# Kernel optimization log

Measured on AMD Instinct MI355X. Metric: run time of the kernel, lower is better.

Reference implementation:

```python
import jax, jax.numpy as jnp
import numpy as np

_SIGMA = 1.5
_K1 = 0.01
_K2 = 0.03
_WINDOW_SIZE = 11
_N_CHANNELS = 3
_VALUE_RANGE = 1.0
_WEIGHTS = np.array([0.0448, 0.2856, 0.3001, 0.2363, 0.1333], dtype=np.float32)


def create_window(window_size: int, n_channels: int) -> jnp.ndarray:
    # 2D Gaussian kernel, normalized to sum 1, expanded to depthwise (C,1,ws,ws)
    coords = np.arange(window_size, dtype=np.float32) - (window_size - 1) / 2.0
    g = np.exp(-(coords ** 2) / (2.0 * _SIGMA ** 2))
    g = g / g.sum()
    k2d = np.outer(g, g).astype(np.float32)  # (ws, ws), sums to 1
    window = np.broadcast_to(k2d[None, None], (n_channels, 1, window_size, window_size))
    return jnp.asarray(window)


def _dwconv(x, window):
    # depthwise valid conv, NCHW / OIHW
    c = x.shape[1]
    return jax.lax.conv_general_dilated(
        x, window, window_strides=(1, 1), padding='VALID',
        dimension_numbers=('NCHW', 'OIHW', 'NCHW'), feature_group_count=c)


def _avg_pool2(x):
    # torch F.avg_pool2d(kernel=2, stride=2, padding=(H%2, W%2), count_include_pad=True)
    ph = x.shape[-2] % 2
    pw = x.shape[-1] % 2
    s = jax.lax.reduce_window(
        x, 0.0, jax.lax.add, window_dimensions=(1, 1, 2, 2),
        window_strides=(1, 1, 2, 2), padding=((0, 0), (0, 0), (ph, ph), (pw, pw)))
    return s * 0.25


def ssim_per_channel(x, y, window, value_range):
    mu_x = _dwconv(x, window)
    mu_y = _dwconv(y, window)
    mu_x_sq = mu_x ** 2
    mu_y_sq = mu_y ** 2
    mu_xy = mu_x * mu_y
    sigma_x_sq = _dwconv(x * x, window) - mu_x_sq
    sigma_y_sq = _dwconv(y * y, window) - mu_y_sq
    sigma_xy = _dwconv(x * y, window) - mu_xy
    c1 = (_K1 * value_range) ** 2
    c2 = (_K2 * value_range) ** 2
    cs_map = (2.0 * sigma_xy + c2) / (sigma_x_sq + sigma_y_sq + c2)
    ssim_map = (2.0 * mu_xy + c1) / (mu_x_sq + mu_y_sq + c1) * cs_map
    return ssim_map.mean(axis=(-1, -2)), cs_map.mean(axis=(-1, -2))  # (N, C) each


def msssim_per_channel(x, y, window, weights, value_range):
    n_scales = weights.shape[0]
    mcs = []
    for i in range(n_scales):
        if i > 0:
            x = _avg_pool2(x)
            y = _avg_pool2(y)
        ssim_val, cs = ssim_per_channel(x, y, window, value_range)
        mcs.append(jax.nn.relu(cs))
    stacked = jnp.stack(mcs[:-1] + [ssim_val], axis=0)  # (M, N, C)
    stacked = stacked ** weights[:, None, None]
    return jnp.prod(stacked, axis=0)  # (N, C)


def setup_inputs() -> dict:
    key = jax.random.key(0)
    k1, k2 = jax.random.split(key)
    N, C, H, W = 16, 3, 512, 512
    x = jax.random.uniform(k1, (N, C, H, W), dtype=jnp.float32)
    # target correlated with input (realistic distorted-image pair)
    noise = jax.random.uniform(k2, (N, C, H, W), dtype=jnp.float32)
    y = jnp.clip(0.9 * x + 0.1 * noise, 0.0, 1.0)
    window = create_window(_WINDOW_SIZE, _N_CHANNELS)
    weights = jnp.asarray(_WEIGHTS)
    return {"x": x, "y": y, "window": window, "weights": weights}


def reference(x, y, window, weights):
    l = msssim_per_channel(x, y, window, weights, _VALUE_RANGE).mean(axis=-1)  # (N,)
    return l.mean()  # reduction='mean' -> scalar
```

## Files before the change

kernel.cpp:

```cpp
#include <hip/hip_runtime.h>

#define HALO 10
#define SWD 76

typedef float v2f __attribute__((ext_vector_type(2)));

#define G0 0.00102838f
#define G1 0.00759871f
#define G2 0.03600077f
#define G3 0.10936069f
#define G4 0.21300556f
#define G5 0.26601176f
#define G6 G4
#define G7 G3
#define G8 G2
#define G9 G1
#define G10 G0

#define HT(QA, QB, W0, W1)                                          \
    { v2f p0; p0.x = QA.x; p0.y = QB.x;                              \
      hm += p0 * (W0); hs += p0 * p0 * (W0); hc += QA.x * QB.x * (W0);\
      v2f p1; p1.x = QA.y; p1.y = QB.y;                              \
      hm += p1 * (W1); hs += p1 * p1 * (W1); hc += QA.y * QB.y * (W1); }

__global__ __launch_bounds__(256, 3) void ssim_wave_kernel(
    const float* __restrict__ x, const float* __restrict__ y,
    float* __restrict__ xo, float* __restrict__ yo,
    float* __restrict__ acc, int H, int W, int ROWS, int do_pool)
{
    const int OH = H - HALO, OW = W - HALO;
    const int nc = blockIdx.z;
    const int tid = threadIdx.x;
    const int wave = tid >> 6, lane = tid & 63;
    const int col0 = blockIdx.x * 64;
    const int r0 = (blockIdx.y * 4 + wave) * ROWS;

    const int c = col0 + lane;
    const bool colvalid = (c < OW);
    const int cl = min(c, W - 1);
    const int chalo = min(col0 + 64 + lane, W - 1);

    const int n_out = min(ROWS, OH - r0);
    const int poolrows = do_pool ? min(ROWS, H - r0) : 0;
    const int n_iter = max(n_out > 0 ? n_out + HALO : 0, poolrows);

    const float* xp = x + (size_t)nc * H * W;
    const float* yp = y + (size_t)nc * H * W;

    __shared__ float sA[4][SWD];
    __shared__ float sB[4][SWD];
    float* myA = sA[wave];
    float* myB = sB[wave];

    const int par = lane & 1;
    const float w2_0  = par ? 0.f : G0;
    const float w2_1  = par ? G0  : G1;
    const float w2_2  = par ? G1  : G2;
    const float w2_3  = par ? G2  : G3;
    const float w2_4  = par ? G3  : G4;
    const float w2_5  = par ? G4  : G5;
    const float w2_6  = par ? G5  : G6;
    const float w2_7  = par ? G6  : G7;
    const float w2_8  = par ? G7  : G8;
    const float w2_9  = par ? G8  : G9;
    const float w2_10 = par ? G9  : G10;
    const float w2_11 = par ? G10 : 0.f;
    const int e = lane & ~1;

    v2f Hm0={0.f,0.f}, Hm1=Hm0, Hm2=Hm0, Hm3=Hm0, Hm4=Hm0, Hm5=Hm0,
        Hm6=Hm0, Hm7=Hm0, Hm8=Hm0, Hm9=Hm0, Hm10=Hm0;
    v2f Hs0=Hm0, Hs1=Hm0, Hs2=Hm0, Hs3=Hm0, Hs4=Hm0, Hs5=Hm0,
        Hs6=Hm0, Hs7=Hm0, Hs8=Hm0, Hs9=Hm0, Hs10=Hm0;
    float Hc0=0.f, Hc1=0.f, Hc2=0.f, Hc3=0.f, Hc4=0.f, Hc5=0.f,
          Hc6=0.f, Hc7=0.f, Hc8=0.f, Hc9=0.f, Hc10=0.f;

    float ssim_sum = 0.f, cs_sum = 0.f;

    float vx = 0.f, vy = 0.f, hxv = 0.f, hyv = 0.f;
    float prevx = 0.f, prevy = 0.f;

    const int Wo = W >> 1;
    float* xop = xo + (size_t)nc * (H >> 1) * Wo + (col0 >> 1);
    float* yop = yo + (size_t)nc * (H >> 1) * Wo + (col0 >> 1);

    if (n_iter > 0) {
        {
            const float* rx = xp + (size_t)r0 * W;
            const float* ry = yp + (size_t)r0 * W;
            vx = rx[cl]; vy = ry[cl];
            if (lane < HALO) { hxv = rx[chalo]; hyv = ry[chalo]; }
        }
        const int NI = ((n_iter + 10) / 11) * 11;
        for (int ii = 0; ii < NI; ii += 11) {
#pragma unroll
            for (int u = 0; u < 11; ++u) {
                const int i = ii + u;

                if (do_pool && i < poolrows) {
                    float sx2 = vx + __shfl_xor(vx, 1, 64);
                    float sy2 = vy + __shfl_xor(vy, 1, 64);
                    if (i & 1) {
                        if (par == 0) {
                            const int pr = (r0 + i) >> 1;
                            xop[(size_t)pr * Wo + (lane >> 1)] = 0.25f * (prevx + sx2);
                            yop[(size_t)pr * Wo + (lane >> 1)] = 0.25f * (prevy + sy2);
                        }
                    } else { prevx = sx2; prevy = sy2; }
                }

                myA[lane] = vx; myB[lane] = vy;
                if (lane < HALO) { myA[64 + lane] = hxv; myB[64 + lane] = hyv; }

                {
                    const int rr = min(r0 + i + 1, H - 1);
                    const float* rx = xp + (size_t)rr * W;
                    const float* ry = yp + (size_t)rr * W;
                    vx = rx[cl]; vy = ry[cl];
                    if (lane < HALO) { hxv = rx[chalo]; hyv = ry[chalo]; }
                }

                const v2f* pa = (const v2f*)&myA[e];
                const v2f* pb = (const v2f*)&myB[e];
                const v2f qa0 = pa[0], qa1 = pa[1], qa2 = pa[2],
                          qa3 = pa[3], qa4 = pa[4], qa5 = pa[5];
                const v2f qb0 = pb[0], qb1 = pb[1], qb2 = pb[2],
                          qb3 = pb[3], qb4 = pb[4], qb5 = pb[5];
                v2f hm = {0.f, 0.f}, hs = {0.f, 0.f};
                float hc = 0.f;
                HT(qa0, qb0, w2_0,  w2_1)
                HT(qa1, qb1, w2_2,  w2_3)
                HT(qa2, qb2, w2_4,  w2_5)
                HT(qa3, qb3, w2_6,  w2_7)
                HT(qa4, qb4, w2_8,  w2_9)
                HT(qa5, qb5, w2_10, w2_11)

                Hm0=Hm1; Hm1=Hm2; Hm2=Hm3; Hm3=Hm4; Hm4=Hm5; Hm5=Hm6;
                Hm6=Hm7; Hm7=Hm8; Hm8=Hm9; Hm9=Hm10; Hm10=hm;
                Hs0=Hs1; Hs1=Hs2; Hs2=Hs3; Hs3=Hs4; Hs4=Hs5; Hs5=Hs6;
                Hs6=Hs7; Hs7=Hs8; Hs8=Hs9; Hs9=Hs10; Hs10=hs;
                Hc0=Hc1; Hc1=Hc2; Hc2=Hc3; Hc3=Hc4; Hc4=Hc5; Hc5=Hc6;
                Hc6=Hc7; Hc7=Hc8; Hc8=Hc9; Hc9=Hc10; Hc10=hc;

                const int o = i - HALO;
                if (o >= 0 && o < n_out && colvalid) {
                    v2f vm = Hm0*G0; vm += Hm1*G1; vm += Hm2*G2; vm += Hm3*G3;
                    vm += Hm4*G4; vm += Hm5*G5; vm += Hm6*G6; vm += Hm7*G7;
                    vm += Hm8*G8; vm += Hm9*G9; vm += Hm10*G10;
                    v2f vs = Hs0*G0; vs += Hs1*G1; vs += Hs2*G2; vs += Hs3*G3;
                    vs += Hs4*G4; vs += Hs5*G5; vs += Hs6*G6; vs += Hs7*G7;
                    vs += Hs8*G8; vs += Hs9*G9; vs += Hs10*G10;
                    float vc = Hc0*G0; vc += Hc1*G1; vc += Hc2*G2; vc += Hc3*G3;
                    vc += Hc4*G4; vc += Hc5*G5; vc += Hc6*G6; vc += Hc7*G7;
                    vc += Hc8*G8; vc += Hc9*G9; vc += Hc10*G10;

                    const float mx = vm.x, my = vm.y;
                    const float mu_x2 = mx * mx, mu_y2 = my * my, mu_xy = mx * my;
                    const float sxq = vs.x - mu_x2, syq = vs.y - mu_y2, sxyv = vc - mu_xy;
                    const float c1 = 1e-4f, c2 = 9e-4f;
                    const float cs = (2.f * sxyv + c2) * __builtin_amdgcn_rcpf(sxq + syq + c2);
                    const float ssim = (2.f * mu_xy + c1) * __builtin_amdgcn_rcpf(mu_x2 + mu_y2 + c1) * cs;
                    ssim_sum += ssim;
                    cs_sum += cs;
                }
            }
        }
    }

#pragma unroll
    for (int off = 32; off > 0; off >>= 1) {
        ssim_sum += __shfl_down(ssim_sum, off, 64);
        cs_sum   += __shfl_down(cs_sum,   off, 64);
    }
    if (lane == 0) {
        atomicAdd(&acc[nc * 2 + 0], ssim_sum);
        atomicAdd(&acc[nc * 2 + 1], cs_sum);
    }
}

__global__ void finalize_kernel(const float* __restrict__ acc,
                                const float* __restrict__ weights,
                                float* __restrict__ out)
{
    int t = threadIdx.x;
    float v = 0.f;
    if (t < 48) {
        float prod = 1.f;
#pragma unroll
        for (int s = 0; s < 5; ++s) {
            int O = (512 >> s) - HALO;
            float inv = 1.f / ((float)O * (float)O);
            float ssim = acc[s * 96 + t * 2 + 0] * inv;
            float cs   = acc[s * 96 + t * 2 + 1] * inv;
            float val = (s < 4) ? fmaxf(cs, 0.f) : ssim;
            prod *= powf(val, weights[s]);
        }
        v = prod;
    }
#pragma unroll
    for (int off = 32; off > 0; off >>= 1) v += __shfl_down(v, off, 64);
    if (t == 0) out[0] = v * (1.f / 48.f);
}

extern "C" void kernel_launch(void* const* d_in, const int* in_sizes, int n_in,
                              void* d_out, int out_size, void* d_ws, size_t ws_size,
                              hipStream_t stream) {
    const float* x = (const float*)d_in[0];
    const float* y = (const float*)d_in[1];
    const float* weights = (const float*)d_in[3];
    float* out = (float*)d_out;
    float* ws = (float*)d_ws;

    float* acc = ws;
    float* xs1 = ws + 512;
    float* ys1 = xs1 + (size_t)48 * 256 * 256;
    float* xs2 = ys1 + (size_t)48 * 256 * 256;
    float* ys2 = xs2 + (size_t)48 * 128 * 128;
    float* xs3 = ys2 + (size_t)48 * 128 * 128;
    float* ys3 = xs3 + (size_t)48 * 64 * 64;
    float* xs4 = ys3 + (size_t)48 * 64 * 64;
    float* ys4 = xs4 + (size_t)48 * 32 * 32;

    hipMemsetAsync(acc, 0, 480 * sizeof(float), stream);

    dim3 blk(256);
    ssim_wave_kernel<<<dim3(8, 2, 48), blk, 0, stream>>>(x, y, xs1, ys1, acc + 0 * 96, 512, 512, 64, 1);
    ssim_wave_kernel<<<dim3(4, 2, 48), blk, 0, stream>>>(xs1, ys1, xs2, ys2, acc + 1 * 96, 256, 256, 32, 1);
    ssim_wave_kernel<<<dim3(2, 2, 48), blk, 0, stream>>>(xs2, ys2, xs3, ys3, acc + 2 * 96, 128, 128, 16, 1);
    ssim_wave_kernel<<<dim3(1, 2, 48), blk, 0, stream>>>(xs3, ys3, xs4, ys4, acc + 3 * 96, 64, 64, 8, 1);
    ssim_wave_kernel<<<dim3(1, 1, 48), blk, 0, stream>>>(xs4, ys4, nullptr, nullptr, acc + 4 * 96, 32, 32, 8, 0);

    finalize_kernel<<<dim3(1), dim3(64), 0, stream>>>(acc, weights, out);
}
```

Before: 286.1 us.

## Process two rows per step in SSIM wave kernel and shrink per-wave row strips

New measurement: 667.7 us. 133% more time.

```diff
diff --git a/kernel.cpp b/kernel.cpp
--- a/kernel.cpp
+++ b/kernel.cpp
@@ -17,13 +17,59 @@
 #define G9 G1
 #define G10 G0
 
-#define HT(QA, QB, W0, W1)                                          \
-    { v2f p0; p0.x = QA.x; p0.y = QB.x;                              \
-      hm += p0 * (W0); hs += p0 * p0 * (W0); hc += QA.x * QB.x * (W0);\
-      v2f p1; p1.x = QA.y; p1.y = QB.y;                              \
-      hm += p1 * (W1); hs += p1 * p1 * (W1); hc += QA.y * QB.y * (W1); }
-
-__global__ __launch_bounds__(256, 3) void ssim_wave_kernel(
+#define HT(QA, QB, W0, W1, HM, HS, HC)                                   \
+    { v2f p0; p0.x = QA.x; p0.y = QB.x;                                   \
+      HM += p0 * (W0); HS += p0 * p0 * (W0); HC += QA.x * QB.x * (W0);    \
+      v2f p1; p1.x = QA.y; p1.y = QB.y;                                   \
+      HM += p1 * (W1); HS += p1 * p1 * (W1); HC += QA.y * QB.y * (W1); }
+
+#define HCONV(AP, BP, HM, HS, HC)                                         \
+    { const v2f* pa = (const v2f*)&(AP)[e];                               \
+      const v2f* pb = (const v2f*)&(BP)[e];                               \
+      const v2f qa0 = pa[0], qa1 = pa[1], qa2 = pa[2],                    \
+                qa3 = pa[3], qa4 = pa[4], qa5 = pa[5];                    \
+      const v2f qb0 = pb[0], qb1 = pb[1], qb2 = pb[2],                    \
+                qb3 = pb[3], qb4 = pb[4], qb5 = pb[5];                    \
+      HM = (v2f){0.f, 0.f}; HS = (v2f){0.f, 0.f}; HC = 0.f;               \
+      HT(qa0, qb0, w2_0,  w2_1,  HM, HS, HC)                              \
+      HT(qa1, qb1, w2_2,  w2_3,  HM, HS, HC)                              \
+      HT(qa2, qb2, w2_4,  w2_5,  HM, HS, HC)                              \
+      HT(qa3, qb3, w2_6,  w2_7,  HM, HS, HC)                              \
+      HT(qa4, qb4, w2_8,  w2_9,  HM, HS, HC)                              \
+      HT(qa5, qb5, w2_10, w2_11, HM, HS, HC) }
+
+#define VSHIFT(NM, NS, NC)                                                \
+    Hm0=Hm1; Hm1=Hm2; Hm2=Hm3; Hm3=Hm4; Hm4=Hm5; Hm5=Hm6;                 \
+    Hm6=Hm7; Hm7=Hm8; Hm8=Hm9; Hm9=Hm10; Hm10=NM;                         \
+    Hs0=Hs1; Hs1=Hs2; Hs2=Hs3; Hs3=Hs4; Hs4=Hs5; Hs5=Hs6;                 \
+    Hs6=Hs7; Hs7=Hs8; Hs8=Hs9; Hs9=Hs10; Hs10=NS;                         \
+    Hc0=Hc1; Hc1=Hc2; Hc2=Hc3; Hc3=Hc4; Hc4=Hc5; Hc5=Hc6;                 \
+    Hc6=Hc7; Hc7=Hc8; Hc8=Hc9; Hc9=Hc10; Hc10=NC;
+
+#define VOUT(OROW)                                                        \
+    if ((OROW) >= 0 && (OROW) < n_out && colvalid) {                      \
+        v2f vm = Hm0*G0; vm += Hm1*G1; vm += Hm2*G2; vm += Hm3*G3;        \
+        vm += Hm4*G4; vm += Hm5*G5; vm += Hm6*G6; vm += Hm7*G7;           \
+        vm += Hm8*G8; vm += Hm9*G9; vm += Hm10*G10;                       \
+        v2f vs = Hs0*G0; vs += Hs1*G1; vs += Hs2*G2; vs += Hs3*G3;        \
+        vs += Hs4*G4; vs += Hs5*G5; vs += Hs6*G6; vs += Hs7*G7;           \
+        vs += Hs8*G8; vs += Hs9*G9; vs += Hs10*G10;                       \
+        float vc = Hc0*G0; vc += Hc1*G1; vc += Hc2*G2; vc += Hc3*G3;      \
+        vc += Hc4*G4; vc += Hc5*G5; vc += Hc6*G6; vc += Hc7*G7;           \
+        vc += Hc8*G8; vc += Hc9*G9; vc += Hc10*G10;                       \
+        const float mx = vm.x, my = vm.y;                                 \
+        const float mu_x2 = mx * mx, mu_y2 = my * my, mu_xy = mx * my;    \
+        const float sxq = vs.x - mu_x2, syq = vs.y - mu_y2;               \
+        const float sxyv = vc - mu_xy;                                    \
+        const float c1 = 1e-4f, c2 = 9e-4f;                               \
+        const float cs = (2.f * sxyv + c2)                                \
+                       * __builtin_amdgcn_rcpf(sxq + syq + c2);           \
+        const float ssim = (2.f * mu_xy + c1)                             \
+                         * __builtin_amdgcn_rcpf(mu_x2 + mu_y2 + c1) * cs;\
+        ssim_sum += ssim; cs_sum += cs;                                   \
+    }
+
+__global__ __launch_bounds__(256, 4) void ssim_wave_kernel(
     const float* __restrict__ x, const float* __restrict__ y,
     float* __restrict__ xo, float* __restrict__ yo,
     float* __restrict__ acc, int H, int W, int ROWS, int do_pool)
@@ -47,10 +93,10 @@
     const float* xp = x + (size_t)nc * H * W;
     const float* yp = y + (size_t)nc * H * W;
 
-    __shared__ float sA[4][SWD];
-    __shared__ float sB[4][SWD];
-    float* myA = sA[wave];
-    float* myB = sB[wave];
+    __shared__ float sA[4][2 * SWD];
+    __shared__ float sB[4][2 * SWD];
+    float* A0 = sA[wave];        float* B0 = sB[wave];
+    float* A1 = sA[wave] + SWD;  float* B1 = sB[wave] + SWD;
 
     const int par = lane & 1;
     const float w2_0  = par ? 0.f : G0;
@@ -76,8 +122,8 @@
 
     float ssim_sum = 0.f, cs_sum = 0.f;
 
-    float vx = 0.f, vy = 0.f, hxv = 0.f, hyv = 0.f;
-    float prevx = 0.f, prevy = 0.f;
+    float cx0=0.f, cy0=0.f, hx0=0.f, hy0=0.f;
+    float cx1=0.f, cy1=0.f, hx1=0.f, hy1=0.f;
 
     const int Wo = W >> 1;
     float* xop = xo + (size_t)nc * (H >> 1) * Wo + (col0 >> 1);
@@ -85,83 +131,74 @@
 
     if (n_iter > 0) {
         {
-            const float* rx = xp + (size_t)r0 * W;
-            const float* ry = yp + (size_t)r0 * W;
-            vx = rx[cl]; vy = ry[cl];
-            if (lane < HALO) { hxv = rx[chalo]; hyv = ry[chalo]; }
+            const float* rx0 = xp + (size_t)r0 * W;
+            const float* ry0 = yp + (size_t)r0 * W;
+            const int r1 = min(r0 + 1, H - 1);
+            const float* rx1 = xp + (size_t)r1 * W;
+            const float* ry1 = yp + (size_t)r1 * W;
+            cx0 = rx0[cl]; cy0 = ry0[cl];
+            cx1 = rx1[cl]; cy1 = ry1[cl];
+            if (lane < HALO) {
+                hx0 = rx0[chalo]; hy0 = ry0[chalo];
+                hx1 = rx1[chalo]; hy1 = ry1[chalo];
+            }
         }
-        const int NI = ((n_iter + 10) / 11) * 11;
-        for (int ii = 0; ii < NI; ii += 11) {
+        const int steps = (n_iter + 1) >> 1;
+        const int nouter = (steps + 10) / 11;
+        for (int t = 0; t < nouter; ++t) {
+            const int ib = t * 22;
 #pragma unroll
             for (int u = 0; u < 11; ++u) {
-                const int i = ii + u;
+                const int i = ib + 2 * u;
 
                 if (do_pool && i < poolrows) {
-                    float sx2 = vx + __shfl_xor(vx, 1, 64);
-                    float sy2 = vy + __shfl_xor(vy, 1, 64);
-                    if (i & 1) {
-                        if (par == 0) {
-                            const int pr = (r0 + i) >> 1;
-                            xop[(size_t)pr * Wo + (lane >> 1)] = 0.25f * (prevx + sx2);
-                            yop[(size_t)pr * Wo + (lane >> 1)] = 0.25f * (prevy + sy2);
-                        }
-                    } else { prevx = sx2; prevy = sy2; }
+                    const float s0x = cx0 + __shfl_xor(cx0, 1, 64);
+                    const float s0y = cy0 + __shfl_xor(cy0, 1, 64);
+                    const float s1x = cx1 + __shfl_xor(cx1, 1, 64);
+                    const float s1y = cy1 + __shfl_xor(cy1, 1, 64);
+                    if (par == 0) {
+                        const int pr = (r0 + i) >> 1;
+                        xop[(size_t)pr * Wo + (lane >> 1)] = 0.25f * (s0x + s1x);
+                        yop[(size_t)pr * Wo + (lane >> 1)] = 0.25f * (s0y + s1y);
+                    }
                 }
 
-                myA[lane] = vx; myB[lane] = vy;
-                if (lane < HALO) { myA[64 + lane] = hxv; myB[64 + lane] = hyv; }
-
+                A0[lane] = cx0; B0[lane] = cy0;
+                A1[lane] = cx1; B1[lane] = cy1;
+                if (lane < HALO) {
+                    A0[64 + lane] = hx0; B0[64 + lane] = hy0;
+                    A1[64 + lane] = hx1; B1[64 + lane] = hy1;
+                }
+
+                float nx0, ny0, nhx0 = 0.f, nhy0 = 0.f;
+                float nx1, ny1, nhx1 = 0.f, nhy1 = 0.f;
                 {
-                    const int rr = min(r0 + i + 1, H - 1);
-                    const float* rx = xp + (size_t)rr * W;
-                    const float* ry = yp + (size_t)rr * W;
-                    vx = rx[cl]; vy = ry[cl];
-                    if (lane < HALO) { hxv = rx[chalo]; hyv = ry[chalo]; }
+                    const int r2 = min(r0 + i + 2, H - 1);
+                    const int r3 = min(r0 + i + 3, H - 1);
+                    const float* rx2 = xp + (size_t)r2 * W;
+                    const float* ry2 = yp + (size_t)r2 * W;
+                    const float* rx3 = xp + (size_t)r3 * W;
+                    const float* ry3 = yp + (size_t)r3 * W;
+                    nx0 = rx2[cl]; ny0 = ry2[cl];
+                    nx1 = rx3[cl]; ny1 = ry3[cl];
+                    if (lane < HALO) {
+                        nhx0 = rx2[chalo]; nhy0 = ry2[chalo];
+                        nhx1 = rx3[chalo]; nhy1 = ry3[chalo];
+                    }
                 }
 
-                const v2f* pa = (const v2f*)&myA[e];
-                const v2f* pb = (const v2f*)&myB[e];
-                const v2f qa0 = pa[0], qa1 = pa[1], qa2 = pa[2],
-                          qa3 = pa[3], qa4 = pa[4], qa5 = pa[5];
-                const v2f qb0 = pb[0], qb1 = pb[1], qb2 = pb[2],
-                          qb3 = pb[3], qb4 = pb[4], qb5 = pb[5];
-                v2f hm = {0.f, 0.f}, hs = {0.f, 0.f};
-                float hc = 0.f;
-                HT(qa0, qb0, w2_0,  w2_1)
-                HT(qa1, qb1, w2_2,  w2_3)
-                HT(qa2, qb2, w2_4,  w2_5)
-                HT(qa3, qb3, w2_6,  w2_7)
-                HT(qa4, qb4, w2_8,  w2_9)
-                HT(qa5, qb5, w2_10, w2_11)
-
-                Hm0=Hm1; Hm1=Hm2; Hm2=Hm3; Hm3=Hm4; Hm4=Hm5; Hm5=Hm6;
-                Hm6=Hm7; Hm7=Hm8; Hm8=Hm9; Hm9=Hm10; Hm10=hm;
-                Hs0=Hs1; Hs1=Hs2; Hs2=Hs3; Hs3=Hs4; Hs4=Hs5; Hs5=Hs6;
-                Hs6=Hs7; Hs7=Hs8; Hs8=Hs9; Hs9=Hs10; Hs10=hs;
-                Hc0=Hc1; Hc1=Hc2; Hc2=Hc3; Hc3=Hc4; Hc4=Hc5; Hc5=Hc6;
-                Hc6=Hc7; Hc7=Hc8; Hc8=Hc9; Hc9=Hc10; Hc10=hc;
-
-                const int o = i - HALO;
-                if (o >= 0 && o < n_out && colvalid) {
-                    v2f vm = Hm0*G0; vm += Hm1*G1; vm += Hm2*G2; vm += Hm3*G3;
-                    vm += Hm4*G4; vm += Hm5*G5; vm += Hm6*G6; vm += Hm7*G7;
-                    vm += Hm8*G8; vm += Hm9*G9; vm += Hm10*G10;
-                    v2f vs = Hs0*G0; vs += Hs1*G1; vs += Hs2*G2; vs += Hs3*G3;
-                    vs += Hs4*G4; vs += Hs5*G5; vs += Hs6*G6; vs += Hs7*G7;
-                    vs += Hs8*G8; vs += Hs9*G9; vs += Hs10*G10;
-                    float vc = Hc0*G0; vc += Hc1*G1; vc += Hc2*G2; vc += Hc3*G3;
-                    vc += Hc4*G4; vc += Hc5*G5; vc += Hc6*G6; vc += Hc7*G7;
-                    vc += Hc8*G8; vc += Hc9*G9; vc += Hc10*G10;
-
-                    const float mx = vm.x, my = vm.y;
-                    const float mu_x2 = mx * mx, mu_y2 = my * my, mu_xy = mx * my;
-                    const float sxq = vs.x - mu_x2, syq = vs.y - mu_y2, sxyv = vc - mu_xy;
-                    const float c1 = 1e-4f, c2 = 9e-4f;
-                    const float cs = (2.f * sxyv + c2) * __builtin_amdgcn_rcpf(sxq + syq + c2);
-                    const float ssim = (2.f * mu_xy + c1) * __builtin_amdgcn_rcpf(mu_x2 + mu_y2 + c1) * cs;
-                    ssim_sum += ssim;
-                    cs_sum += cs;
-                }
+                v2f hma, hsa; float hca;
+                v2f hmb, hsb; float hcb;
+                HCONV(A0, B0, hma, hsa, hca)
+                HCONV(A1, B1, hmb, hsb, hcb)
+
+                VSHIFT(hma, hsa, hca)
+                VOUT(i - HALO)
+                VSHIFT(hmb, hsb, hcb)
+                VOUT(i - HALO + 1)
+
+                cx0 = nx0; cy0 = ny0; hx0 = nhx0; hy0 = nhy0;
+                cx1 = nx1; cy1 = ny1; hx1 = nhx1; hy1 = nhy1;
             }
         }
     }
@@ -223,11 +260,11 @@
     hipMemsetAsync(acc, 0, 480 * sizeof(float), stream);
 
     dim3 blk(256);
-    ssim_wave_kernel<<<dim3(8, 2, 48), blk, 0, stream>>>(x, y, xs1, ys1, acc + 0 * 96, 512, 512, 64, 1);
-    ssim_wave_kernel<<<dim3(4, 2, 48), blk, 0, stream>>>(xs1, ys1, xs2, ys2, acc + 1 * 96, 256, 256, 32, 1);
-    ssim_wave_kernel<<<dim3(2, 2, 48), blk, 0, stream>>>(xs2, ys2, xs3, ys3, acc + 2 * 96, 128, 128, 16, 1);
+    ssim_wave_kernel<<<dim3(8, 4, 48), blk, 0, stream>>>(x, y, xs1, ys1, acc + 0 * 96, 512, 512, 32, 1);
+    ssim_wave_kernel<<<dim3(4, 4, 48), blk, 0, stream>>>(xs1, ys1, xs2, ys2, acc + 1 * 96, 256, 256, 16, 1);
+    ssim_wave_kernel<<<dim3(2, 4, 48), blk, 0, stream>>>(xs2, ys2, xs3, ys3, acc + 2 * 96, 128, 128, 8, 1);
     ssim_wave_kernel<<<dim3(1, 2, 48), blk, 0, stream>>>(xs3, ys3, xs4, ys4, acc + 3 * 96, 64, 64, 8, 1);
-    ssim_wave_kernel<<<dim3(1, 1, 48), blk, 0, stream>>>(xs4, ys4, nullptr, nullptr, acc + 4 * 96, 32, 32, 8, 0);
+    ssim_wave_kernel<<<dim3(1, 1, 48), blk, 0, stream>>>(xs4, ys4, nullptr, nullptr, acc + 4 * 96, 32, 32, 6, 0);
 
     finalize_kernel<<<dim3(1), dim3(64), 0, stream>>>(acc, weights, out);
 }
```
